# Optimization experiments

Measured on AMD Instinct MI355X. Metric: run time of the kernel, lower is better.

Reference implementation:

```python
import jax, jax.numpy as jnp
import numpy as np

NUM_HEADS = 12  # per init_kwargs


def setup_inputs() -> dict:
    key = jax.random.key(0)
    k1, k2, k3 = jax.random.split(key, 3)
    B, H, W, D = 1, 64, 64, 768
    x = jax.random.normal(k1, (B, H, W, D), dtype=jnp.float32)
    # torch nn.Linear weights are [out, in]; small init keeps softmax well-conditioned
    w_qkv = jax.random.normal(k2, (3 * D, D), dtype=jnp.float32) * 0.02
    w_proj = jax.random.normal(k3, (D, D), dtype=jnp.float32) * 0.02
    b_proj = jnp.zeros((D,), dtype=jnp.float32)
    return {"x": x, "w_qkv": w_qkv, "w_proj": w_proj, "b_proj": b_proj}


def reference(x, w_qkv, w_proj, b_proj):
    B, H, W, D = x.shape
    S = H * W
    nh = NUM_HEADS
    hd = D // nh
    scale = hd ** (-0.5)
    # qkv: [B, S, 3, nh, hd] -> q,k,v each [B, nh, S, hd]
    qkv = jnp.einsum('bhwd,ed->bhwe', x, w_qkv).reshape(B, S, 3, nh, hd)
    qkv = jnp.transpose(qkv, (2, 0, 3, 1, 4))
    q, k, v = qkv[0], qkv[1], qkv[2]
    # full O(S^2) attention matrix, as in the original module
    wei = jnp.einsum('bnqd,bnkd->bnqk', q * scale, k)
    wei = jax.nn.softmax(wei, axis=-1)
    # att_drop omitted (eval mode / deterministic baseline)
    out = jnp.einsum('bnqk,bnkd->bnqd', wei, v)  # [B, nh, S, hd]
    # [B, nh, H, W, hd] -> [B, H, W, nh*hd]
    out = jnp.transpose(out.reshape(B, nh, H, W, hd), (0, 2, 3, 1, 4)).reshape(B, H, W, D)
    proj = jnp.einsum('bhwd,ed->bhwe', out, w_proj) + b_proj
    return proj
```

## Files before the change

### kernel.cpp

```cpp
#include <hip/hip_runtime.h>
#include <hip/hip_bf16.h>
#include <math.h>

typedef short s16x8 __attribute__((ext_vector_type(8)));
typedef unsigned u32x2 __attribute__((ext_vector_type(2)));
typedef unsigned u32x4 __attribute__((ext_vector_type(4)));
typedef float f32x4 __attribute__((ext_vector_type(4)));
typedef float f32x16 __attribute__((ext_vector_type(16)));
typedef __hip_bfloat16 bf16;

#define GLD16(g, l)                                                        \
  __builtin_amdgcn_global_load_lds(                                        \
      (const __attribute__((address_space(1))) void*)(g),                  \
      (__attribute__((address_space(3))) void*)(l), 16, 0, 0)

#define MFMA16(a, b, c) __builtin_amdgcn_mfma_f32_16x16x32_bf16((a), (b), (c), 0, 0, 0)
#define MFMA32(a, b, c) __builtin_amdgcn_mfma_f32_32x32x16_bf16((a), (b), (c), 0, 0, 0)

static constexpr int kS = 4096;
static constexpr int kD = 768;
static constexpr int kNH = 12;
static constexpr int kHD = 64;
static constexpr int kNE = 2304;
static constexpr int kNS = 3;

static __device__ __forceinline__ float bf2f(short s) {
  union { unsigned u; float f; } x;
  x.u = ((unsigned)(unsigned short)s) << 16;
  return x.f;
}

static __device__ __forceinline__ unsigned pk_bf16(float lo, float hi) {
  float2 f2;
  f2.x = lo;
  f2.y = hi;
  __hip_bfloat162 h2 = __float22bfloat162_rn(f2);
  return (unsigned)__bfloat16_as_ushort(h2.x) |
         ((unsigned)__bfloat16_as_ushort(h2.y) << 16);
}

static constexpr int kNX8 = kS * kD / 8;
static constexpr int kNWq8 = kNE * kD / 8;
static constexpr int kNWp8 = kD * kD / 8;

__global__ __launch_bounds__(256)
void k_cvt3(const float* __restrict__ x, const float* __restrict__ wq,
            const float* __restrict__ wp, bf16* __restrict__ xb,
            bf16* __restrict__ wqb, bf16* __restrict__ wpb) {
  int i = blockIdx.x * 256 + threadIdx.x;
  const float* src;
  short* dst;
  if (i < kNX8) {
    src = x; dst = (short*)xb;
  } else if (i < kNX8 + kNWq8) {
    i -= kNX8; src = wq; dst = (short*)wqb;
  } else {
    i -= kNX8 + kNWq8; if (i >= kNWp8) return;
    src = wp; dst = (short*)wpb;
  }
  const f32x4 a = *(const f32x4*)(src + i * 8);
  const f32x4 b = *(const f32x4*)(src + i * 8 + 4);
  s16x8 o;
#pragma unroll
  for (int j = 0; j < 4; ++j) {
    o[j] = (short)__bfloat16_as_ushort(__float2bfloat16(a[j]));
    o[j + 4] = (short)__bfloat16_as_ushort(__float2bfloat16(b[j]));
  }
  *(s16x8*)(dst + i * 8) = o;
}

__global__ __launch_bounds__(256, 2)
void k_qkv(const bf16* __restrict__ X, const bf16* __restrict__ W,
           bf16* __restrict__ Qw, bf16* __restrict__ Kw, bf16* __restrict__ Vw) {
  __shared__ __align__(16) short As[2][128 * 32];
  __shared__ __align__(16) short Bs[2][128 * 32];
  const int tid = threadIdx.x;
  const int wv = tid >> 6, ln = tid & 63;
  const int r = ln & 15, kq = ln >> 4;
  const int bm = blockIdx.x * 128;
  const int bn = blockIdx.y * 128;
  const int wr = wv >> 1, wc = wv & 1;
  const short* Xs = (const short*)X;
  const short* Ws = (const short*)W;

  f32x4 acc[4][4] = {};

  const int c0 = wv * 128 + ln, c1 = c0 + 64;
  const int ra0 = c0 >> 2, ka0 = c0 & 3;
  const int ra1 = c1 >> 2, ka1 = c1 & 3;
  const int off0 = wv * 1024, off1 = off0 + 512;
  const short* gA0 = Xs + (bm + ra0) * kD + ka0 * 8;
  const short* gA1 = Xs + (bm + ra1) * kD + ka1 * 8;
  const short* gB0 = Ws + (bn + ra0) * kD + ka0 * 8;
  const short* gB1 = Ws + (bn + ra1) * kD + ka1 * 8;

  GLD16(gA0, &As[0][off0]);
  GLD16(gA1, &As[0][off1]);
  GLD16(gB0, &Bs[0][off0]);
  GLD16(gB1, &Bs[0][off1]);
  __syncthreads();

  const int NT = kD / 32;
  for (int t = 0; t < NT; ++t) {
    const short* aCur = As[t & 1];
    const short* bCur = Bs[t & 1];
    if (t + 1 < NT) {
      const int k1 = (t + 1) * 32;
      short* aN = As[(t + 1) & 1];
      short* bN = Bs[(t + 1) & 1];
      GLD16(gA0 + k1, aN + off0);
      GLD16(gA1 + k1, aN + off1);
      GLD16(gB0 + k1, bN + off0);
      GLD16(gB1 + k1, bN + off1);
    }
    s16x8 a[4], b[4];
#pragma unroll
    for (int i = 0; i < 4; ++i)
      a[i] = *(const s16x8*)(aCur + (wr * 64 + i * 16 + r) * 32 + kq * 8);
#pragma unroll
    for (int j = 0; j < 4; ++j)
      b[j] = *(const s16x8*)(bCur + (wc * 64 + j * 16 + r) * 32 + kq * 8);
#pragma unroll
    for (int i = 0; i < 4; ++i)
#pragma unroll
      for (int j = 0; j < 4; ++j) acc[i][j] = MFMA16(a[i], b[j], acc[i][j]);
    __syncthreads();
  }

  const int which = bn / kD;
  bf16* dst = (which == 0) ? Qw : (which == 1) ? Kw : Vw;
  const float scl = (which == 0) ? 0.125f : 1.0f;
  const int ebase = bn - which * kD + wc * 64;
#pragma unroll
  for (int j = 0; j < 4; ++j) {
    const int e = ebase + j * 16 + r;
    const int h = e >> 6, d = e & 63;
#pragma unroll
    for (int i = 0; i < 4; ++i) {
      const int srow = bm + wr * 64 + i * 16 + kq * 4;
#pragma unroll
      for (int rr = 0; rr < 4; ++rr)
        dst[(h * kS + srow + rr) * kHD + d] = __float2bfloat16(acc[i][j][rr] * scl);
    }
  }
}

__global__ __launch_bounds__(256, 2)
void k_vt(const bf16* __restrict__ Vw, bf16* __restrict__ Vt) {
  __shared__ __align__(16) short L[64 * 72];
  const int h = blockIdx.y, st = blockIdx.x;
  const int t = threadIdx.x;
  const short* src = (const short*)Vw + (h * kS + st * 64) * kHD;
  short* dstb = (short*)Vt + h * kHD * kS;
#pragma unroll
  for (int u = 0; u < 2; ++u) {
    const int c = u * 256 + t;
    const int row = c >> 3, ch = c & 7;
    *(s16x8*)(L + row * 72 + ch * 8) = *(const s16x8*)(src + row * kHD + ch * 8);
  }
  __syncthreads();
#pragma unroll
  for (int u = 0; u < 2; ++u) {
    const int c = u * 256 + t;
    const int d = c >> 3, ch = c & 7;
    s16x8 v;
#pragma unroll
    for (int j = 0; j < 8; ++j) v[j] = L[(ch * 8 + j) * 72 + d];
    *(s16x8*)(dstb + d * kS + st * 64 + ch * 8) = v;
  }
}

__global__ __launch_bounds__(256, 5)
void k_attn(const bf16* __restrict__ Qw, const bf16* __restrict__ Kw,
            const bf16* __restrict__ Vt, bf16* __restrict__ Opart,
            float* __restrict__ Lpart) {
  __shared__ __align__(16) short Ks[2][64 * 64];
  __shared__ __align__(16) short Vs[2][64 * 64];
  const int tid = threadIdx.x;
  const int wv = tid >> 6, ln = tid & 63;
  const int qh = wv >> 1;
  const int kvh = wv & 1;
  const int col = ln & 31;
  const int lh = ln >> 5;

  const int wg = blockIdx.x;
  const int p = (wg & 7) >> 1;
  const int b = ((wg >> 3) << 1) | (wg & 1);
  const int hh = 3 * p + b / 192;
  const int rem = b % 192;
  const int qb = rem / 3;
  const int j = rem % 3;
  const int q0 = qb * 64;
  const int pidx = (hh * 64 + qb) * kNS + j;
  const int t0 = (j * 64) / 3;
  const int t1 = ((j + 1) * 64) / 3;

  const short* Qh = (const short*)Qw + ((size_t)hh * kS + q0 + qh * 32) * kHD;
  const short* Kh = (const short*)Kw + (size_t)hh * kS * kHD;
  const short* Vh = (const short*)Vt + (size_t)hh * kHD * kS;

  s16x8 bq[4];
#pragma unroll
  for (int kb = 0; kb < 4; ++kb)
    bq[kb] = *(const s16x8*)(Qh + col * kHD + kb * 16 + lh * 8);

  f32x16 o[2] = {};
  float lp = 0.f;

  int ldso[2];
  const short* gK[2];
  const short* gV[2];
#pragma unroll
  for (int u = 0; u < 2; ++u) {
    const int c = u * 256 + tid;
    const int kr = c >> 3, g = (c & 7) ^ (kr & 7);
    ldso[u] = c * 8;
    gK[u] = Kh + kr * kHD + g * 8;
    gV[u] = Vh + kr * kS + g * 8;
  }

#pragma unroll
  for (int u = 0; u < 2; ++u) {
    GLD16(gK[u] + t0 * 64 * kHD, &Ks[0][ldso[u]]);
    GLD16(gV[u] + t0 * 64, &Vs[0][ldso[u]]);
  }
  __syncthreads();

  for (int kt = t0; kt < t1; ++kt) {
    const int i = kt - t0;
    const short* ksCur = Ks[i & 1];
    const short* vsCur = Vs[i & 1];
    if (kt + 1 < t1) {
      short* ksN = Ks[(i + 1) & 1];
      short* vsN = Vs[(i + 1) & 1];
      const int dk = (kt + 1) * 64 * kHD;
      const int dv = (kt + 1) * 64;
#pragma unroll
      for (int u = 0; u < 2; ++u) {
        GLD16(gK[u] + dk, ksN + ldso[u]);
        GLD16(gV[u] + dv, vsN + ldso[u]);
      }
    }

    f32x16 z = {};
    const int krow = kvh * 32 + col;
    const int ksw = krow & 7;
    __builtin_amdgcn_s_setprio(1);
#pragma unroll
    for (int kb = 0; kb < 4; ++kb) {
      const int ch = ((kb << 1) + lh) ^ ksw;
      s16x8 ak = *(const s16x8*)(ksCur + krow * 64 + ch * 8);
      z = MFMA32(ak, bq[kb], z);
    }
    __builtin_amdgcn_s_setprio(0);

    float pv[16];
#pragma unroll
    for (int g = 0; g < 16; ++g) {
      pv[g] = __expf(z[g]);
      lp += pv[g];
    }
    unsigned own[8];
#pragma unroll
    for (int m = 0; m < 8; ++m)
      own[m] = pk_bf16(pv[2 * m], pv[2 * m + 1]);

    __builtin_amdgcn_s_setprio(1);
#pragma unroll
    for (int kvk = 0; kvk < 2; ++kvk) {
      u32x2 sA = __builtin_amdgcn_permlane32_swap(own[4 * kvk + 0], own[4 * kvk + 2], false, false);
      u32x2 sB = __builtin_amdgcn_permlane32_swap(own[4 * kvk + 1], own[4 * kvk + 3], false, false);
      u32x4 apv;
      apv[0] = sA[0];
      apv[1] = sB[0];
      apv[2] = sA[1];
      apv[3] = sB[1];
      const s16x8 ap = __builtin_bit_cast(s16x8, apv);
      const int kvg = kvh * 2 + kvk;
#pragma unroll
      for (int db = 0; db < 2; ++db) {
        const int vrow = db * 32 + col;
        const int ch = ((kvg << 1) + lh) ^ (vrow & 7);
        s16x8 vb = *(const s16x8*)(vsCur + vrow * 64 + ch * 8);
        o[db] = MFMA32(ap, vb, o[db]);
      }
    }
    __builtin_amdgcn_s_setprio(0);
    __syncthreads();
  }

  lp += __shfl_xor(lp, 32);
  float* Of = (float*)Ks;
  float* Lf = (float*)Vs;

  if (kvh == 1) {
#pragma unroll
    for (int db = 0; db < 2; ++db)
#pragma unroll
      for (int g = 0; g < 16; ++g) {
        const int qoff = (g & 3) + 8 * (g >> 2) + 4 * lh;
        Of[(qh * 32 + qoff) * 64 + db * 32 + col] = o[db][g];
      }
    if (lh == 0) Lf[qh * 32 + col] = lp;
  }
  __syncthreads();
  if (kvh == 0) {
    lp += Lf[qh * 32 + col];
    if (lh == 0) Lpart[pidx * 64 + qh * 32 + col] = lp;
    short* Ob = (short*)Opart + (size_t)pidx * 4096;
#pragma unroll
    for (int db = 0; db < 2; ++db)
#pragma unroll
      for (int g = 0; g < 16; ++g) {
        const int qoff = (g & 3) + 8 * (g >> 2) + 4 * lh;
        const float val = o[db][g] + Of[(qh * 32 + qoff) * 64 + db * 32 + col];
        Ob[(qh * 32 + qoff) * 64 + db * 32 + col] =
            (short)__bfloat16_as_ushort(__float2bfloat16(val));
      }
  }
}

__global__ __launch_bounds__(256)
void k_comb(bf16* __restrict__ Opart, const float* __restrict__ Lpart) {
  const int blk = blockIdx.x;
  const int t = threadIdx.x;
  const int q = t >> 2;
  const int dg = t & 3;
  const int p0 = blk * kNS;
  const float inv = 1.0f / (Lpart[p0 * 64 + q] + Lpart[(p0 + 1) * 64 + q] +
                            Lpart[(p0 + 2) * 64 + q]);
  short* s0 = (short*)Opart + (size_t)p0 * 4096 + q * 64 + dg * 16;
  const short* s1 = s0 + 4096;
  const short* s2 = s0 + 8192;
#pragma unroll
  for (int jj = 0; jj < 2; ++jj) {
    const s16x8 a = *(const s16x8*)(s0 + jj * 8);
    const s16x8 bb = *(const s16x8*)(s1 + jj * 8);
    const s16x8 cc = *(const s16x8*)(s2 + jj * 8);
    s16x8 r;
#pragma unroll
    for (int e = 0; e < 8; ++e) {
      const float v = (bf2f(a[e]) + bf2f(bb[e]) + bf2f(cc[e])) * inv;
      r[e] = (short)__bfloat16_as_ushort(__float2bfloat16(v));
    }
    *(s16x8*)(s0 + jj * 8) = r;
  }
}

__global__ __launch_bounds__(256, 3)
void k_proj(const bf16* __restrict__ Opart, const bf16* __restrict__ W,
            const float* __restrict__ Bias, float* __restrict__ Out) {
  __shared__ __align__(16) short As[2][64 * 32];
  __shared__ __align__(16) short Bs[2][64 * 32];
  const int tid = threadIdx.x;
  const int wv = tid >> 6, ln = tid & 63;
  const int r = ln & 15, kq = ln >> 4;
  const int bm = blockIdx.x * 64;
  const int bn = blockIdx.y * 64;
  const int wr = wv >> 1, wc = wv & 1;
  const short* Asrc = (const short*)Opart;
  const short* Wsrc = (const short*)W;

  f32x4 acc[2][2] = {};
  const int c = wv * 64 + ln;
  const int ra = c >> 2, ka = c & 3;
  const int off = wv * 512;
  const int s = bm + ra;
  const int baseQ = (s >> 6) * (kNS * 4096) + (s & 63) * 64;
  const short* gB = Wsrc + (bn + ra) * kD + ka * 8;

  GLD16(Asrc + baseQ + ka * 8, &As[0][off]);
  GLD16(gB, &Bs[0][off]);
  __syncthreads();

  const int NT = kD / 32;
  for (int t = 0; t < NT; ++t) {
    const short* aCur = As[t & 1];
    const short* bCur = Bs[t & 1];
    if (t + 1 < NT) {
      const int tn = t + 1;
      const int aoff = baseQ + (tn >> 1) * (64 * kNS * 4096) +
                       ((tn & 1) * 32 + ka * 8);
      GLD16(Asrc + aoff, &As[tn & 1][off]);
      GLD16(gB + tn * 32, &Bs[tn & 1][off]);
    }
    s16x8 a[2], b[2];
#pragma unroll
    for (int i = 0; i < 2; ++i)
      a[i] = *(const s16x8*)(aCur + (wr * 32 + i * 16 + r) * 32 + kq * 8);
#pragma unroll
    for (int jj = 0; jj < 2; ++jj)
      b[jj] = *(const s16x8*)(bCur + (wc * 32 + jj * 16 + r) * 32 + kq * 8);
#pragma unroll
    for (int i = 0; i < 2; ++i)
#pragma unroll
      for (int jj = 0; jj < 2; ++jj) acc[i][jj] = MFMA16(a[i], b[jj], acc[i][jj]);
    __syncthreads();
  }
#pragma unroll
  for (int jj = 0; jj < 2; ++jj) {
    const int e = bn + wc * 32 + jj * 16 + r;
    const float bv = Bias[e];
#pragma unroll
    for (int i = 0; i < 2; ++i) {
      const int srow = bm + wr * 32 + i * 16 + kq * 4;
#pragma unroll
      for (int rr = 0; rr < 4; ++rr)
        Out[(srow + rr) * kD + e] = acc[i][jj][rr] + bv;
    }
  }
}

extern "C" void kernel_launch(void* const* d_in, const int* in_sizes, int n_in,
                              void* d_out, int out_size, void* d_ws, size_t ws_size,
                              hipStream_t stream) {
  const float* x = (const float*)d_in[0];
  const float* w_qkv = (const float*)d_in[1];
  const float* w_proj = (const float*)d_in[2];
  const float* b_proj = (const float*)d_in[3];
  float* out = (float*)d_out;

  const size_t HS = (size_t)kNH * kS * kHD;
  const int nX = kS * kD;
  const int nWq = kNE * kD;
  const int nWp = kD * kD;

  bf16* Wpb = (bf16*)d_ws;
  bf16* Qw = Wpb + nWp;
  bf16* Kw = Qw + HS;
  bf16* Vt = Kw + HS;
  bf16* Xb = Vt + HS;
  bf16* Wqb = Xb + nX;
  bf16* Vw = Wqb + nWq;
  bf16* Opart = Xb;
  float* Lpart = (float*)((short*)Opart + (size_t)kNS * 768 * 4096);

  const int totalC = kNX8 + kNWq8 + kNWp8;
  k_cvt3<<<(totalC + 255) / 256, 256, 0, stream>>>(x, w_qkv, w_proj, Xb, Wqb, Wpb);

  k_qkv<<<dim3(kS / 128, kNE / 128), 256, 0, stream>>>(Xb, Wqb, Qw, Kw, Vw);
  k_vt<<<dim3(kS / 64, kNH), 256, 0, stream>>>(Vw, Vt);
  k_attn<<<dim3(kNS * (kS / 64) * kNH), 256, 0, stream>>>(Qw, Kw, Vt, Opart, Lpart);
  k_comb<<<dim3((kS / 64) * kNH), 256, 0, stream>>>(Opart, Lpart);
  k_proj<<<dim3(kS / 64, kD / 64), 256, 0, stream>>>(Opart, Wpb, b_proj, out);
}
```

Measured before the change: 132.4 us.

## Split attention KV range into two halves and truncate probabilities to bf16

Changes the split-KV attention from three uneven KV chunks per query block to two equal chunks of 32 tiles each, with index math reduced to shifts and masks, and the combine kernel now sums two partials. Probability packing switches from round-to-nearest bf16 conversion to a byte-permute truncation. Fewer splits means fewer partial writes and less combine traffic, but also fewer workgroups and a longer serial loop per workgroup. Truncation adds a small numerical bias in P.

```diff
diff --git a/kernel.cpp b/kernel.cpp
--- a/kernel.cpp
+++ b/kernel.cpp
@@ -22,21 +22,12 @@
 static constexpr int kNH = 12;
 static constexpr int kHD = 64;
 static constexpr int kNE = 2304;
-static constexpr int kNS = 3;
+static constexpr int kNS = 2;
 
 static __device__ __forceinline__ float bf2f(short s) {
   union { unsigned u; float f; } x;
   x.u = ((unsigned)(unsigned short)s) << 16;
   return x.f;
-}
-
-static __device__ __forceinline__ unsigned pk_bf16(float lo, float hi) {
-  float2 f2;
-  f2.x = lo;
-  f2.y = hi;
-  __hip_bfloat162 h2 = __float22bfloat162_rn(f2);
-  return (unsigned)__bfloat16_as_ushort(h2.x) |
-         ((unsigned)__bfloat16_as_ushort(h2.y) << 16);
 }
 
 static constexpr int kNX8 = kS * kD / 8;
@@ -186,18 +177,16 @@
   const int wg = blockIdx.x;
   const int p = (wg & 7) >> 1;
   const int b = ((wg >> 3) << 1) | (wg & 1);
-  const int hh = 3 * p + b / 192;
-  const int rem = b % 192;
-  const int qb = rem / 3;
-  const int j = rem % 3;
+  const int hh = 3 * p + (b >> 7);
+  const int rem = b & 127;
+  const int qb = rem >> 1;
+  const int j = rem & 1;
   const int q0 = qb * 64;
   const int pidx = (hh * 64 + qb) * kNS + j;
-  const int t0 = (j * 64) / 3;
-  const int t1 = ((j + 1) * 64) / 3;
 
   const short* Qh = (const short*)Qw + ((size_t)hh * kS + q0 + qh * 32) * kHD;
-  const short* Kh = (const short*)Kw + (size_t)hh * kS * kHD;
-  const short* Vh = (const short*)Vt + (size_t)hh * kHD * kS;
+  const short* Kh = (const short*)Kw + (size_t)hh * kS * kHD + (size_t)j * 2048 * kHD;
+  const short* Vh = (const short*)Vt + (size_t)hh * kHD * kS + j * 2048;
 
   s16x8 bq[4];
 #pragma unroll
@@ -221,18 +210,18 @@
 
 #pragma unroll
   for (int u = 0; u < 2; ++u) {
-    GLD16(gK[u] + t0 * 64 * kHD, &Ks[0][ldso[u]]);
-    GLD16(gV[u] + t0 * 64, &Vs[0][ldso[u]]);
+    GLD16(gK[u], &Ks[0][ldso[u]]);
+    GLD16(gV[u], &Vs[0][ldso[u]]);
   }
   __syncthreads();
 
-  for (int kt = t0; kt < t1; ++kt) {
-    const int i = kt - t0;
-    const short* ksCur = Ks[i & 1];
-    const short* vsCur = Vs[i & 1];
-    if (kt + 1 < t1) {
-      short* ksN = Ks[(i + 1) & 1];
-      short* vsN = Vs[(i + 1) & 1];
+  const int NT2 = 32;
+  for (int kt = 0; kt < NT2; ++kt) {
+    const short* ksCur = Ks[kt & 1];
+    const short* vsCur = Vs[kt & 1];
+    if (kt + 1 < NT2) {
+      short* ksN = Ks[(kt + 1) & 1];
+      short* vsN = Vs[(kt + 1) & 1];
       const int dk = (kt + 1) * 64 * kHD;
       const int dv = (kt + 1) * 64;
 #pragma unroll
@@ -262,8 +251,11 @@
     }
     unsigned own[8];
 #pragma unroll
-    for (int m = 0; m < 8; ++m)
-      own[m] = pk_bf16(pv[2 * m], pv[2 * m + 1]);
+    for (int m = 0; m < 8; ++m) {
+      const unsigned f0 = __builtin_bit_cast(unsigned, pv[2 * m]);
+      const unsigned f1 = __builtin_bit_cast(unsigned, pv[2 * m + 1]);
+      own[m] = __builtin_amdgcn_perm(f1, f0, 0x07060302u);
+    }
 
     __builtin_amdgcn_s_setprio(1);
 #pragma unroll
@@ -327,20 +319,17 @@
   const int q = t >> 2;
   const int dg = t & 3;
   const int p0 = blk * kNS;
-  const float inv = 1.0f / (Lpart[p0 * 64 + q] + Lpart[(p0 + 1) * 64 + q] +
-                            Lpart[(p0 + 2) * 64 + q]);
+  const float inv = 1.0f / (Lpart[p0 * 64 + q] + Lpart[(p0 + 1) * 64 + q]);
   short* s0 = (short*)Opart + (size_t)p0 * 4096 + q * 64 + dg * 16;
   const short* s1 = s0 + 4096;
-  const short* s2 = s0 + 8192;
 #pragma unroll
   for (int jj = 0; jj < 2; ++jj) {
     const s16x8 a = *(const s16x8*)(s0 + jj * 8);
     const s16x8 bb = *(const s16x8*)(s1 + jj * 8);
-    const s16x8 cc = *(const s16x8*)(s2 + jj * 8);
     s16x8 r;
 #pragma unroll
     for (int e = 0; e < 8; ++e) {
-      const float v = (bf2f(a[e]) + bf2f(bb[e]) + bf2f(cc[e])) * inv;
+      const float v = (bf2f(a[e]) + bf2f(bb[e])) * inv;
       r[e] = (short)__bfloat16_as_ushort(__float2bfloat16(v));
     }
     *(s16x8*)(s0 + jj * 8) = r;
```

Result: faster. 126.8 us (median of 3 runs) (-4.2%).
